# Performance work log

Measured on AMD Instinct MI355X. Metric: run time of the kernel, lower is better.

## Reference

```python
import jax, jax.numpy as jnp
import numpy as np

H_DIM = 1024
NUM_HEADS = 16
HEAD_DIM = H_DIM // NUM_HEADS
EPS = 1e-5


def rms_norm(x, w, eps=EPS):
    var = jnp.mean(jnp.square(x), axis=-1, keepdims=True)
    return x * jax.lax.rsqrt(var + eps) * w


def setup_inputs() -> dict:
    key = jax.random.key(0)
    ks = jax.random.split(key, 8)
    B, S = 2, 2048
    x = jax.random.normal(ks[0], (B, S, H_DIM), dtype=jnp.float32)
    # learned params (orthogonal init approximated by scaled normal for a correctness baseline)
    qkv_w = jax.random.normal(ks[1], (3 * H_DIM, H_DIM), dtype=jnp.float32) / np.sqrt(H_DIM)
    gate_w = jax.random.normal(ks[2], (NUM_HEADS, H_DIM), dtype=jnp.float32) / np.sqrt(H_DIM)
    o_w = jax.random.normal(ks[3], (H_DIM, H_DIM), dtype=jnp.float32) / np.sqrt(H_DIM)
    prenorm_w = jnp.ones((H_DIM,), dtype=jnp.float32)
    q_norm_w = jnp.ones((HEAD_DIM,), dtype=jnp.float32)
    k_norm_w = jnp.ones((HEAD_DIM,), dtype=jnp.float32)
    return {"x": x, "prenorm_w": prenorm_w, "qkv_w": qkv_w, "gate_w": gate_w,
            "o_w": o_w, "q_norm_w": q_norm_w, "k_norm_w": k_norm_w}


def reference(x, prenorm_w, qkv_w, gate_w, o_w, q_norm_w, k_norm_w):
    B, S, D = x.shape
    residual = x
    xn = rms_norm(x, prenorm_w)                                   # [B,S,D]
    qkv = jnp.einsum('bsd,ed->bse', xn, qkv_w)                    # [B,S,3D]
    qkv = qkv.reshape(B, S, 3, NUM_HEADS, HEAD_DIM)
    gate = jnp.einsum('bsd,hd->bsh', xn, gate_w)                  # [B,S,H]
    q, k, v = qkv[:, :, 0], qkv[:, :, 1], qkv[:, :, 2]            # [B,S,H,hd]
    q = rms_norm(q, q_norm_w)
    k = rms_norm(k, k_norm_w)
    scale = 1.0 / np.sqrt(HEAD_DIM).astype(np.float32)
    scores = jnp.einsum('bqhd,bkhd->bhqk', q, k) * scale          # [B,H,S,S]
    attn = jax.nn.softmax(scores, axis=-1)
    out = jnp.einsum('bhqk,bkhd->bhqd', attn, v)                  # [B,H,S,hd]
    out = out * jax.nn.sigmoid(gate).transpose(0, 2, 1)[..., None]
    out = out.transpose(0, 2, 1, 3).reshape(B, S, D)              # [B,S,D]
    return jnp.einsum('bsd,ed->bse', out, o_w) + residual
```

## Files before the change

kernel.cpp:

```cpp
#include <hip/hip_runtime.h>
#include <math.h>

typedef __bf16 bf16x8 __attribute__((ext_vector_type(8)));
typedef float f32x4 __attribute__((ext_vector_type(4)));
typedef float f32x16 __attribute__((ext_vector_type(16)));
typedef unsigned int uint2v __attribute__((ext_vector_type(2)));
typedef unsigned int uint4v __attribute__((ext_vector_type(4)));
typedef unsigned short ushort_t;

#define SEQ 2048
#define MROWS 4096
#define EPS 1e-5f
#define QKS 3200
#define LOG2E 1.4426950408889634f
#define SMAX_B2 17.32f

__device__ __forceinline__ float bf2f(ushort_t u) {
  union { unsigned int i; float f; } c; c.i = ((unsigned int)u) << 16; return c.f;
}
__device__ __forceinline__ ushort_t f2bf(float f) {
  union { unsigned int i; float f; } c; c.f = f;
  unsigned int i = c.i;
  unsigned int r = i + 0x7fffu + ((i >> 16) & 1u);
  return (ushort_t)(r >> 16);
}
__device__ __forceinline__ ushort_t f2bf_fast(float f) {
  union { __bf16 b; ushort_t u; } cv; cv.b = (__bf16)f; return cv.u;
}

__device__ __forceinline__ float exp2_raw(float x) {
  float r; asm("v_exp_f32 %0, %1" : "=v"(r) : "v"(x)); return r;
}

#define CVTPK(d, a, b) asm("v_cvt_pk_bf16_f32 %0, %1, %2" : "=v"(d) : "v"(a), "v"(b))

__device__ __forceinline__ void plane_swap(unsigned int &a, unsigned int &b) {
#if __has_builtin(__builtin_amdgcn_permlane32_swap)
  uint2v r = __builtin_amdgcn_permlane32_swap(a, b, 0, 0);
  a = r.x; b = r.y;
#else
  unsigned int sa = (unsigned int)__shfl_xor((int)a, 32);
  unsigned int sb = (unsigned int)__shfl_xor((int)b, 32);
  int hi = (int)((threadIdx.x & 63) >> 5);
  unsigned int na = hi ? sb : a;
  unsigned int nb = hi ? b : sa;
  a = na; b = nb;
#endif
}

__device__ __forceinline__ void softmax_pack(const f32x16 &stv, float &lp,
                                             uint4v &Fa, uint4v &Fb) {
  float p[16];
  #pragma unroll
  for (int r = 0; r < 16; ++r) p[r] = exp2_raw(stv[r] - SMAX_B2);
  float s0 = (p[0] + p[1]) + (p[2] + p[3]);
  float s1 = (p[4] + p[5]) + (p[6] + p[7]);
  float s2 = (p[8] + p[9]) + (p[10] + p[11]);
  float s3 = (p[12] + p[13]) + (p[14] + p[15]);
  lp += (s0 + s1) + (s2 + s3);
  unsigned int X00, X01, X10, X11, X20, X21, X30, X31;
  CVTPK(X00, p[0], p[1]);   CVTPK(X01, p[2], p[3]);
  CVTPK(X10, p[4], p[5]);   CVTPK(X11, p[6], p[7]);
  CVTPK(X20, p[8], p[9]);   CVTPK(X21, p[10], p[11]);
  CVTPK(X30, p[12], p[13]); CVTPK(X31, p[14], p[15]);
  plane_swap(X00, X10); plane_swap(X01, X11);
  plane_swap(X20, X30); plane_swap(X21, X31);
  Fa.x = X00; Fa.y = X01; Fa.z = X10; Fa.w = X11;
  Fb.x = X20; Fb.y = X21; Fb.z = X30; Fb.w = X31;
}

__device__ __forceinline__ float wave_sum(float v) {
  #pragma unroll
  for (int off = 32; off > 0; off >>= 1) v += __shfl_xor(v, off);
  return v;
}

__global__ void detect_kernel(const unsigned int* __restrict__ xraw, int* __restrict__ flag) {
  int tid = threadIdx.x;
  int cnt = 0;
  for (int i = tid; i < 4096; i += 256) {
    unsigned int e = (xraw[i] >> 7) & 0xFFu;
    cnt += (e >= 100u && e <= 150u) ? 1 : 0;
  }
  __shared__ int sred[256];
  sred[tid] = cnt;
  __syncthreads();
  for (int s = 128; s > 0; s >>= 1) {
    if (tid < s) sred[tid] += sred[tid + s];
    __syncthreads();
  }
  if (tid == 0) flag[0] = (sred[0] > 2048) ? 1 : 0;
}

__global__ void prep_kernel(const void* __restrict__ qkvw_in, const void* __restrict__ gw_in,
                            const void* __restrict__ ow_in, const void* __restrict__ pw_in,
                            const void* __restrict__ qn_in, const void* __restrict__ kn_in,
                            ushort_t* __restrict__ Wcat, ushort_t* __restrict__ ow,
                            float* __restrict__ pwf, float* __restrict__ qnf,
                            float* __restrict__ knf, const int* __restrict__ flag) {
  int bid = blockIdx.x, tid = threadIdx.x;
  int bf = *flag;
  if (bid < 12288) {
    int i = bid * 256 + tid;
    Wcat[i] = bf ? ((const ushort_t*)qkvw_in)[i] : f2bf(((const float*)qkvw_in)[i]);
  } else if (bid < 12352) {
    int i = (bid - 12288) * 256 + tid;
    Wcat[3072 * 1024 + i] = bf ? ((const ushort_t*)gw_in)[i] : f2bf(((const float*)gw_in)[i]);
  } else if (bid < 16448) {
    int i = (bid - 12352) * 256 + tid;
    ow[i] = bf ? ((const ushort_t*)ow_in)[i] : f2bf(((const float*)ow_in)[i]);
  } else {
    for (int i = tid; i < 1024; i += 256)
      pwf[i] = bf ? bf2f(((const ushort_t*)pw_in)[i]) : ((const float*)pw_in)[i];
    if (tid < 64) {
      qnf[tid] = bf ? bf2f(((const ushort_t*)qn_in)[tid]) : ((const float*)qn_in)[tid];
      knf[tid] = bf ? bf2f(((const ushort_t*)kn_in)[tid]) : ((const float*)kn_in)[tid];
    }
  }
}

__global__ void prenorm_kernel(const void* __restrict__ xraw,
                               const float* __restrict__ w,
                               ushort_t* __restrict__ xn,
                               const int* __restrict__ flag) {
  int row = blockIdx.x;
  int tid = threadIdx.x;
  float4 u;
  if (*flag) {
    ushort4 s = ((const ushort4*)xraw)[row * 256 + tid];
    u.x = bf2f(s.x); u.y = bf2f(s.y); u.z = bf2f(s.z); u.w = bf2f(s.w);
  } else {
    u = ((const float4*)xraw)[row * 256 + tid];
  }
  float ss = u.x*u.x + u.y*u.y + u.z*u.z + u.w*u.w;
  ss = wave_sum(ss);
  __shared__ float red[4];
  if ((tid & 63) == 0) red[tid >> 6] = ss;
  __syncthreads();
  float total = red[0] + red[1] + red[2] + red[3];
  float inv = rsqrtf(total * (1.0f / 1024.0f) + EPS);
  float4 wu = ((const float4*)w)[tid];
  ushort4 o;
  o.x = f2bf(u.x * inv * wu.x);
  o.y = f2bf(u.y * inv * wu.y);
  o.z = f2bf(u.z * inv * wu.z);
  o.w = f2bf(u.w * inv * wu.w);
  ((ushort4*)(xn + (long long)row * 1024))[tid] = o;
}

__device__ __forceinline__ void gll16(const ushort_t* g, ushort_t* l) {
  __builtin_amdgcn_global_load_lds(
      (const __attribute__((address_space(1))) unsigned int*)g,
      (__attribute__((address_space(3))) unsigned int*)l, 16, 0, 0);
}

__global__ void gemm_qkv_fused(const ushort_t* __restrict__ A, const ushort_t* __restrict__ B,
                               ushort_t* __restrict__ C, float* __restrict__ gate,
                               const float* __restrict__ qw, const float* __restrict__ kw) {
  __shared__ ushort_t As[128 * 32];
  __shared__ ushort_t Bs[128 * 32];
  int tid = threadIdx.x, wave = tid >> 6, lane = tid & 63;
  int m_blk = blockIdx.y * 128, n_blk = blockIdx.x * 128;
  int wm = (wave & 1) * 64, wn = (wave >> 1) * 64;
  int g = lane >> 4, c = lane & 15;
  int arow = lane >> 2;
  int akc = (lane & 3) << 3;
  f32x4 acc[4][4] = {};
  for (int kt = 0; kt < 1024; kt += 32) {
    #pragma unroll
    for (int i = 0; i < 2; ++i) {
      int rbase = (i * 4 + wave) * 16;
      gll16(A + (long long)(m_blk + rbase + arow) * 1024 + kt + akc, &As[rbase * 32]);
      gll16(B + (long long)(n_blk + rbase + arow) * 1024 + kt + akc, &Bs[rbase * 32]);
    }
    __syncthreads();
    bf16x8 af[4], bfr[4];
    #pragma unroll
    for (int mi = 0; mi < 4; ++mi)
      af[mi] = *(const bf16x8*)&As[(wm + mi * 16 + c) * 32 + (g << 3)];
    #pragma unroll
    for (int ni = 0; ni < 4; ++ni)
      bfr[ni] = *(const bf16x8*)&Bs[(wn + ni * 16 + c) * 32 + (g << 3)];
    #pragma unroll
    for (int mi = 0; mi < 4; ++mi)
      #pragma unroll
      for (int ni = 0; ni < 4; ++ni)
        acc[mi][ni] = __builtin_amdgcn_mfma_f32_16x16x32_bf16(af[mi], bfr[ni], acc[mi][ni], 0, 0, 0);
    __syncthreads();
  }
  int col_base = n_blk + wn;
  if (col_base < 2048) {
    int isk = col_base >= 1024;
    float scale = isk ? 1.0f : (0.125f * LOG2E);
    const float* nw = isk ? kw : qw;
    float w[4];
    #pragma unroll
    for (int ni = 0; ni < 4; ++ni) w[ni] = nw[ni * 16 + c];
    #pragma unroll
    for (int mi = 0; mi < 4; ++mi)
      #pragma unroll
      for (int r = 0; r < 4; ++r) {
        float ss = 0.f;
        #pragma unroll
        for (int ni = 0; ni < 4; ++ni) ss += acc[mi][ni][r] * acc[mi][ni][r];
        #pragma unroll
        for (int off = 8; off > 0; off >>= 1) ss += __shfl_xor(ss, off);
        float inv = rsqrtf(ss * (1.0f / 64.0f) + EPS) * scale;
        int row = m_blk + wm + mi * 16 + g * 4 + r;
        #pragma unroll
        for (int ni = 0; ni < 4; ++ni)
          C[(long long)row * QKS + col_base + ni * 16 + c] = f2bf(acc[mi][ni][r] * inv * w[ni]);
      }
  } else if (col_base < 3072) {
    #pragma unroll
    for (int mi = 0; mi < 4; ++mi)
      #pragma unroll
      for (int r = 0; r < 4; ++r) {
        int row = m_blk + wm + mi * 16 + g * 4 + r;
        #pragma unroll
        for (int ni = 0; ni < 4; ++ni)
          C[(long long)row * QKS + col_base + ni * 16 + c] = f2bf(acc[mi][ni][r]);
      }
  } else if (col_base == 3072) {
    #pragma unroll
    for (int mi = 0; mi < 4; ++mi)
      #pragma unroll
      for (int r = 0; r < 4; ++r) {
        int row = m_blk + wm + mi * 16 + g * 4 + r;
        float v = acc[mi][0][r];
        gate[(long long)row * 16 + c] = 1.0f / (1.0f + __expf(-v));
      }
  }
}

__global__ void gemm_tiled(const ushort_t* __restrict__ A, const ushort_t* __restrict__ B,
                           void* __restrict__ Cv, const void* __restrict__ res,
                           const int* __restrict__ flag,
                           int K, int lda, int ldb, int ldc) {
  __shared__ ushort_t As[128 * 32];
  __shared__ ushort_t Bs[128 * 32];
  int tid = threadIdx.x, wave = tid >> 6, lane = tid & 63;
  int m_blk = blockIdx.y * 128, n_blk = blockIdx.x * 128;
  int wm = (wave & 1) * 64, wn = (wave >> 1) * 64;
  int g = lane >> 4, c = lane & 15;
  int arow = lane >> 2;
  int akc = (lane & 3) << 3;
  f32x4 acc[4][4] = {};
  for (int kt = 0; kt < K; kt += 32) {
    #pragma unroll
    for (int i = 0; i < 2; ++i) {
      int rbase = (i * 4 + wave) * 16;
      gll16(A + (long long)(m_blk + rbase + arow) * lda + kt + akc, &As[rbase * 32]);
      gll16(B + (long long)(n_blk + rbase + arow) * ldb + kt + akc, &Bs[rbase * 32]);
    }
    __syncthreads();
    bf16x8 af[4], bfr[4];
    #pragma unroll
    for (int mi = 0; mi < 4; ++mi)
      af[mi] = *(const bf16x8*)&As[(wm + mi * 16 + c) * 32 + (g << 3)];
    #pragma unroll
    for (int ni = 0; ni < 4; ++ni)
      bfr[ni] = *(const bf16x8*)&Bs[(wn + ni * 16 + c) * 32 + (g << 3)];
    #pragma unroll
    for (int mi = 0; mi < 4; ++mi)
      #pragma unroll
      for (int ni = 0; ni < 4; ++ni)
        acc[mi][ni] = __builtin_amdgcn_mfma_f32_16x16x32_bf16(af[mi], bfr[ni], acc[mi][ni], 0, 0, 0);
    __syncthreads();
  }
  int outbf = flag ? *flag : 1;
  #pragma unroll
  for (int mi = 0; mi < 4; ++mi)
    #pragma unroll
    for (int ni = 0; ni < 4; ++ni)
      #pragma unroll
      for (int r = 0; r < 4; ++r) {
        int row = m_blk + wm + mi * 16 + g * 4 + r;
        int col = n_blk + wn + ni * 16 + c;
        long long idx = (long long)row * ldc + col;
        float v = acc[mi][ni][r];
        if (res) v += outbf ? bf2f(((const ushort_t*)res)[idx]) : ((const float*)res)[idx];
        if (outbf) ((ushort_t*)Cv)[idx] = f2bf(v);
        else       ((float*)Cv)[idx] = v;
      }
}

__global__ void vt_kernel(const ushort_t* __restrict__ qkv, ushort_t* __restrict__ Vt) {
  __shared__ ushort_t tile[64][65];
  int s0 = blockIdx.x * 64;
  int bh = blockIdx.y;
  int b = bh >> 4, h = bh & 15;
  const ushort_t* src = qkv + (long long)b * SEQ * QKS + 2048 + h * 64;
  int d = threadIdx.x & 63, srow = threadIdx.x >> 6;
  #pragma unroll
  for (int i = 0; i < 16; ++i) {
    int sl = i * 4 + srow;
    tile[sl][d] = src[(long long)(s0 + sl) * QKS + d];
  }
  __syncthreads();
  ushort_t* dst = Vt + (long long)bh * 64 * SEQ + s0;
  int sl2 = threadIdx.x & 63, drow = threadIdx.x >> 6;
  #pragma unroll
  for (int i = 0; i < 16; ++i) {
    int dd = i * 4 + drow;
    dst[(long long)dd * SEQ + sl2] = tile[sl2][dd];
  }
}

__global__ __launch_bounds__(256, 4)
void flash_kernel(const ushort_t* __restrict__ qkv, const ushort_t* __restrict__ Vt,
                  const float* __restrict__ gate, ushort_t* __restrict__ ao) {
  __shared__ char smem[32768] __attribute__((aligned(16)));
  ushort_t* KsB = (ushort_t*)smem;
  ushort_t* VsB = (ushort_t*)(smem + 16384);
  int tid = threadIdx.x, wave = tid >> 6, lane = tid & 63;
  int al = lane & 31, hi = lane >> 5;
  int fal = (al & 7) ^ ((al >> 3) & 3);
  int qh = wave & 1, kh = wave >> 1;
  int khb = kh * 32;
  int bid = blockIdx.x;
  int xcd = bid & 7, idx = bid >> 3;
  int bh = (xcd << 2) | (idx >> 5);
  int q0 = (idx & 31) * 64;
  int b = bh >> 4, h = bh & 15;
  const ushort_t* qbase = qkv + (long long)b * SEQ * QKS + h * 64;
  const ushort_t* kbase = qbase + 1024;
  const ushort_t* vtbase = Vt + (long long)bh * 64 * SEQ;
  int qrow = q0 + qh * 32 + al;
  bf16x8 bq[4];
  #pragma unroll
  for (int dst = 0; dst < 4; ++dst)
    bq[dst] = *(const bf16x8*)(qbase + (long long)qrow * QKS + dst * 16 + hi * 8);
  asm volatile("s_waitcnt vmcnt(0)"
               :
               : "v"(__builtin_bit_cast(f32x4, bq[0])), "v"(__builtin_bit_cast(f32x4, bq[1])),
                 "v"(__builtin_bit_cast(f32x4, bq[2])), "v"(__builtin_bit_cast(f32x4, bq[3]))
               : "memory");
  f32x16 oac0 = {}, oac1 = {};
  float lp = 0.f;
  int srow = lane >> 3;
  int schk = lane & 7;

  #define STAGE(BUF, S0) do {                                                        \
    int gch = ((schk ^ srow ^ wave) & 7) << 3;                                       \
    int lbo = (BUF) * 4096;                                                          \
    _Pragma("unroll")                                                                \
    for (int tt = 0; tt < 2; ++tt) {                                                 \
      int rb = tt * 32 + wave * 8;                                                   \
      int row = rb + srow;                                                           \
      gll16(kbase + (long long)((S0) + row) * QKS + gch, &KsB[lbo + rb * 64]);       \
      gll16(vtbase + (long long)row * SEQ + (S0) + gch, &VsB[lbo + rb * 64]);        \
    } } while (0)

  #define PIPE_BAR(N) do {                                                           \
    asm volatile("s_waitcnt vmcnt(" #N ")" ::: "memory");                            \
    __builtin_amdgcn_s_barrier();                                                    \
    asm volatile("" ::: "memory");                                                   \
  } while (0)

  #define COMPUTE(BUF) do {                                                          \
    int lbo = (BUF) * 4096;                                                          \
    f32x16 st = {};                                                                  \
    __builtin_amdgcn_s_setprio(1);                                                   \
    _Pragma("unroll")                                                                \
    for (int dst = 0; dst < 4; ++dst) {                                              \
      int ph = (((dst << 1) | hi) ^ fal) << 3;                                       \
      bf16x8 ak = *(const bf16x8*)&KsB[lbo + (khb + al) * 64 + ph];                  \
      st = __builtin_amdgcn_mfma_f32_32x32x16_bf16(ak, bq[dst], st, 0, 0, 0);        \
    }                                                                                \
    __builtin_amdgcn_s_setprio(0);                                                   \
    uint4v Fa, Fb;                                                                   \
    softmax_pack(st, lp, Fa, Fb);                                                    \
    bf16x8 pf0 = __builtin_bit_cast(bf16x8, Fa);                                     \
    bf16x8 pf1 = __builtin_bit_cast(bf16x8, Fb);                                     \
    __builtin_amdgcn_s_setprio(1);                                                   \
    _Pragma("unroll")                                                                \
    for (int kst = 0; kst < 2; ++kst) {                                              \
      int kg = kh * 2 + kst;                                                         \
      int ph = (((kg << 1) | hi) ^ fal) << 3;                                        \
      bf16x8 av0 = *(const bf16x8*)&VsB[lbo + al * 64 + ph];                         \
      bf16x8 av1 = *(const bf16x8*)&VsB[lbo + (32 + al) * 64 + ph];                  \
      bf16x8 pf = kst ? pf1 : pf0;                                                   \
      oac0 = __builtin_amdgcn_mfma_f32_32x32x16_bf16(av0, pf, oac0, 0, 0, 0);        \
      oac1 = __builtin_amdgcn_mfma_f32_32x32x16_bf16(av1, pf, oac1, 0, 0, 0);        \
    }                                                                                \
    __builtin_amdgcn_s_setprio(0);                                                   \
  } while (0)

  STAGE(0, 0);
  for (int it = 0; it < 31; ++it) {
    STAGE((it + 1) & 1, (it + 1) * 64);
    PIPE_BAR(4);
    COMPUTE(it & 1);
    __builtin_amdgcn_s_barrier();
  }
  PIPE_BAR(0);
  COMPUTE(1);
  #undef STAGE
  #undef PIPE_BAR
  #undef COMPUTE

  float ltot = lp + __shfl_xor(lp, 32);
  float* cbuf = (float*)smem;
  float* lbuf = cbuf + 64 * 65;
  int qrl = qh * 32 + al;
  __syncthreads();
  if (kh == 1) {
    #pragma unroll
    for (int r = 0; r < 16; ++r) {
      int d = (r & 3) + 8 * (r >> 2) + 4 * hi;
      cbuf[qrl * 65 + d]      = oac0[r];
      cbuf[qrl * 65 + 32 + d] = oac1[r];
    }
    if (hi == 0) lbuf[qrl] = ltot;
  }
  __syncthreads();
  if (kh == 0) {
    ltot += lbuf[qrl];
    #pragma unroll
    for (int r = 0; r < 16; ++r) {
      int d = (r & 3) + 8 * (r >> 2) + 4 * hi;
      oac0[r] += cbuf[qrl * 65 + d];
      oac1[r] += cbuf[qrl * 65 + 32 + d];
    }
    float sg = gate[(long long)(b * SEQ + qrow) * 16 + h];
    float scale = sg / ltot;
    ushort_t* aobase = ao + (long long)(b * SEQ + qrow) * 1024 + h * 64;
    #define OSTORE(OA, MT) do {                                                      \
      _Pragma("unroll")                                                              \
      for (int tt = 0; tt < 4; ++tt) {                                               \
        ushort4 o;                                                                   \
        o.x = f2bf_fast(OA[4 * tt + 0] * scale);                                     \
        o.y = f2bf_fast(OA[4 * tt + 1] * scale);                                     \
        o.z = f2bf_fast(OA[4 * tt + 2] * scale);                                     \
        o.w = f2bf_fast(OA[4 * tt + 3] * scale);                                     \
        *(ushort4*)(aobase + (MT) * 32 + 8 * tt + 4 * hi) = o;                       \
      } } while (0)
    OSTORE(oac0, 0);
    OSTORE(oac1, 1);
    #undef OSTORE
  }
}

extern "C" void kernel_launch(void* const* d_in, const int* in_sizes, int n_in,
                              void* d_out, int out_size, void* d_ws, size_t ws_size,
                              hipStream_t stream) {
  (void)in_sizes; (void)n_in; (void)out_size; (void)ws_size;
  char* ws = (char*)d_ws;
  ushort_t* Wcat = (ushort_t*)(ws);
  ushort_t* ow   = (ushort_t*)(ws + (7ll << 20));
  float*    pwf  = (float*)   (ws + (9ll << 20));
  float*    qnf  = (float*)   (ws + (9ll << 20) + (8 << 10));
  float*    knf  = (float*)   (ws + (9ll << 20) + (12 << 10));
  int*      flag = (int*)     (ws + (9ll << 20) + (16 << 10));
  float*    gate = (float*)   (ws + (9ll << 20) + (64 << 10));
  ushort_t* xn   = (ushort_t*)(ws + (10ll << 20));
  ushort_t* qkv2 = (ushort_t*)(ws + (18ll << 20));
  ushort_t* Vt   = (ushort_t*)(ws + (44ll << 20));
  ushort_t* ao   = (ushort_t*)(ws + (52ll << 20));

  detect_kernel<<<1, 256, 0, stream>>>((const unsigned int*)d_in[0], flag);
  prep_kernel<<<16449, 256, 0, stream>>>(d_in[2], d_in[3], d_in[4], d_in[1], d_in[5], d_in[6],
                                         Wcat, ow, pwf, qnf, knf, flag);
  prenorm_kernel<<<MROWS, 256, 0, stream>>>(d_in[0], pwf, xn, flag);
  gemm_qkv_fused<<<dim3(25, 32), 256, 0, stream>>>(xn, Wcat, qkv2, gate, qnf, knf);
  vt_kernel<<<dim3(32, 32), 256, 0, stream>>>(qkv2, Vt);
  flash_kernel<<<dim3(1024), 256, 0, stream>>>(qkv2, Vt, gate, ao);
  gemm_tiled<<<dim3(8, 32), 256, 0, stream>>>(ao, ow, d_out, d_in[0], flag,
                                              1024, 1024, 1024, 1024);
}
```

Baseline: 230.6 us.

## Load K/V fragments directly from global into registers, dropping LDS staging

Replaces the LDS double-buffered K/V staging (global-to-LDS loads plus barriers) in the flash attention kernel with per-wave direct global loads of K and transposed-V fragments into registers, double-buffered in software across loop iterations. This removes the LDS traffic and the per-iteration block barriers. The cost is redundant global/L2 reads, since each wave now fetches its own K/V fragments instead of sharing a staged tile. It also raises register pressure, so launch bounds drop from 4 to 3 blocks per CU.

```diff
diff --git a/kernel.cpp b/kernel.cpp
--- a/kernel.cpp
+++ b/kernel.cpp
@@ -307,15 +307,12 @@
   }
 }
 
-__global__ __launch_bounds__(256, 4)
+__global__ __launch_bounds__(256, 3)
 void flash_kernel(const ushort_t* __restrict__ qkv, const ushort_t* __restrict__ Vt,
                   const float* __restrict__ gate, ushort_t* __restrict__ ao) {
-  __shared__ char smem[32768] __attribute__((aligned(16)));
-  ushort_t* KsB = (ushort_t*)smem;
-  ushort_t* VsB = (ushort_t*)(smem + 16384);
+  __shared__ float cbuf[64 * 65 + 64];
   int tid = threadIdx.x, wave = tid >> 6, lane = tid & 63;
   int al = lane & 31, hi = lane >> 5;
-  int fal = (al & 7) ^ ((al >> 3) & 3);
   int qh = wave & 1, kh = wave >> 1;
   int khb = kh * 32;
   int bid = blockIdx.x;
@@ -327,81 +324,71 @@
   const ushort_t* kbase = qbase + 1024;
   const ushort_t* vtbase = Vt + (long long)bh * 64 * SEQ;
   int qrow = q0 + qh * 32 + al;
-  bf16x8 bq[4];
-  #pragma unroll
-  for (int dst = 0; dst < 4; ++dst)
-    bq[dst] = *(const bf16x8*)(qbase + (long long)qrow * QKS + dst * 16 + hi * 8);
-  asm volatile("s_waitcnt vmcnt(0)"
-               :
-               : "v"(__builtin_bit_cast(f32x4, bq[0])), "v"(__builtin_bit_cast(f32x4, bq[1])),
-                 "v"(__builtin_bit_cast(f32x4, bq[2])), "v"(__builtin_bit_cast(f32x4, bq[3]))
-               : "memory");
+  bf16x8 bq0 = *(const bf16x8*)(qbase + (long long)qrow * QKS + 0 * 16 + hi * 8);
+  bf16x8 bq1 = *(const bf16x8*)(qbase + (long long)qrow * QKS + 1 * 16 + hi * 8);
+  bf16x8 bq2 = *(const bf16x8*)(qbase + (long long)qrow * QKS + 2 * 16 + hi * 8);
+  bf16x8 bq3 = *(const bf16x8*)(qbase + (long long)qrow * QKS + 3 * 16 + hi * 8);
   f32x16 oac0 = {}, oac1 = {};
   float lp = 0.f;
-  int srow = lane >> 3;
-  int schk = lane & 7;
-
-  #define STAGE(BUF, S0) do {                                                        \
-    int gch = ((schk ^ srow ^ wave) & 7) << 3;                                       \
-    int lbo = (BUF) * 4096;                                                          \
-    _Pragma("unroll")                                                                \
-    for (int tt = 0; tt < 2; ++tt) {                                                 \
-      int rb = tt * 32 + wave * 8;                                                   \
-      int row = rb + srow;                                                           \
-      gll16(kbase + (long long)((S0) + row) * QKS + gch, &KsB[lbo + rb * 64]);       \
-      gll16(vtbase + (long long)row * SEQ + (S0) + gch, &VsB[lbo + rb * 64]);        \
-    } } while (0)
-
-  #define PIPE_BAR(N) do {                                                           \
-    asm volatile("s_waitcnt vmcnt(" #N ")" ::: "memory");                            \
-    __builtin_amdgcn_s_barrier();                                                    \
-    asm volatile("" ::: "memory");                                                   \
-  } while (0)
-
-  #define COMPUTE(BUF) do {                                                          \
-    int lbo = (BUF) * 4096;                                                          \
+
+  const ushort_t* kp = kbase + (long long)(khb + al) * QKS;
+  const ushort_t* vp = vtbase + (long long)al * SEQ + khb;
+
+  #define KLOAD(K0, K1, K2, K3, PTR) do {                                            \
+    K0 = *(const bf16x8*)((PTR) + 0 * 16 + hi * 8);                                  \
+    K1 = *(const bf16x8*)((PTR) + 1 * 16 + hi * 8);                                  \
+    K2 = *(const bf16x8*)((PTR) + 2 * 16 + hi * 8);                                  \
+    K3 = *(const bf16x8*)((PTR) + 3 * 16 + hi * 8); } while (0)
+  #define VLOAD(V0, V1, V2, V3, PTR) do {                                            \
+    V0 = *(const bf16x8*)((PTR) + hi * 8);                                           \
+    V1 = *(const bf16x8*)((PTR) + 16 + hi * 8);                                      \
+    V2 = *(const bf16x8*)((PTR) + 32 * SEQ + hi * 8);                                \
+    V3 = *(const bf16x8*)((PTR) + 32 * SEQ + 16 + hi * 8); } while (0)
+
+  #define COMPUTE(K0, K1, K2, K3, V0, V1, V2, V3) do {                               \
     f32x16 st = {};                                                                  \
     __builtin_amdgcn_s_setprio(1);                                                   \
-    _Pragma("unroll")                                                                \
-    for (int dst = 0; dst < 4; ++dst) {                                              \
-      int ph = (((dst << 1) | hi) ^ fal) << 3;                                       \
-      bf16x8 ak = *(const bf16x8*)&KsB[lbo + (khb + al) * 64 + ph];                  \
-      st = __builtin_amdgcn_mfma_f32_32x32x16_bf16(ak, bq[dst], st, 0, 0, 0);        \
-    }                                                                                \
+    st = __builtin_amdgcn_mfma_f32_32x32x16_bf16(K0, bq0, st, 0, 0, 0);              \
+    st = __builtin_amdgcn_mfma_f32_32x32x16_bf16(K1, bq1, st, 0, 0, 0);              \
+    st = __builtin_amdgcn_mfma_f32_32x32x16_bf16(K2, bq2, st, 0, 0, 0);              \
+    st = __builtin_amdgcn_mfma_f32_32x32x16_bf16(K3, bq3, st, 0, 0, 0);              \
     __builtin_amdgcn_s_setprio(0);                                                   \
     uint4v Fa, Fb;                                                                   \
     softmax_pack(st, lp, Fa, Fb);                                                    \
     bf16x8 pf0 = __builtin_bit_cast(bf16x8, Fa);                                     \
     bf16x8 pf1 = __builtin_bit_cast(bf16x8, Fb);                                     \
     __builtin_amdgcn_s_setprio(1);                                                   \
-    _Pragma("unroll")                                                                \
-    for (int kst = 0; kst < 2; ++kst) {                                              \
-      int kg = kh * 2 + kst;                                                         \
-      int ph = (((kg << 1) | hi) ^ fal) << 3;                                        \
-      bf16x8 av0 = *(const bf16x8*)&VsB[lbo + al * 64 + ph];                         \
-      bf16x8 av1 = *(const bf16x8*)&VsB[lbo + (32 + al) * 64 + ph];                  \
-      bf16x8 pf = kst ? pf1 : pf0;                                                   \
-      oac0 = __builtin_amdgcn_mfma_f32_32x32x16_bf16(av0, pf, oac0, 0, 0, 0);        \
-      oac1 = __builtin_amdgcn_mfma_f32_32x32x16_bf16(av1, pf, oac1, 0, 0, 0);        \
-    }                                                                                \
+    oac0 = __builtin_amdgcn_mfma_f32_32x32x16_bf16(V0, pf0, oac0, 0, 0, 0);          \
+    oac0 = __builtin_amdgcn_mfma_f32_32x32x16_bf16(V1, pf1, oac0, 0, 0, 0);          \
+    oac1 = __builtin_amdgcn_mfma_f32_32x32x16_bf16(V2, pf0, oac1, 0, 0, 0);          \
+    oac1 = __builtin_amdgcn_mfma_f32_32x32x16_bf16(V3, pf1, oac1, 0, 0, 0);          \
     __builtin_amdgcn_s_setprio(0);                                                   \
   } while (0)
 
-  STAGE(0, 0);
-  for (int it = 0; it < 31; ++it) {
-    STAGE((it + 1) & 1, (it + 1) * 64);
-    PIPE_BAR(4);
-    COMPUTE(it & 1);
-    __builtin_amdgcn_s_barrier();
-  }
-  PIPE_BAR(0);
-  COMPUTE(1);
-  #undef STAGE
-  #undef PIPE_BAR
+  bf16x8 ka0, ka1, ka2, ka3, kb0, kb1, kb2, kb3;
+  bf16x8 va0, va1, va2, va3, vb0, vb1, vb2, vb3;
+
+  KLOAD(ka0, ka1, ka2, ka3, kp);
+  VLOAD(va0, va1, va2, va3, vp);
+  for (int it = 0; it < 32; it += 2) {
+    const ushort_t* kpB = kp + 64 * QKS;
+    const ushort_t* vpB = vp + 64;
+    KLOAD(kb0, kb1, kb2, kb3, kpB);
+    VLOAD(vb0, vb1, vb2, vb3, vpB);
+    COMPUTE(ka0, ka1, ka2, ka3, va0, va1, va2, va3);
+    kp = kpB + 64 * QKS;
+    vp = vpB + 64;
+    if (it + 2 < 32) {
+      KLOAD(ka0, ka1, ka2, ka3, kp);
+      VLOAD(va0, va1, va2, va3, vp);
+    }
+    COMPUTE(kb0, kb1, kb2, kb3, vb0, vb1, vb2, vb3);
+  }
+  #undef KLOAD
+  #undef VLOAD
   #undef COMPUTE
 
   float ltot = lp + __shfl_xor(lp, 32);
-  float* cbuf = (float*)smem;
   float* lbuf = cbuf + 64 * 65;
   int qrl = qh * 32 + al;
   __syncthreads();
```

After: 300.0 us. 30.1% more time.
